# Optimization experiments

Measured on AMD Instinct MI355X. Metric: run time of the kernel, lower is better.

Reference implementation:

```python
import jax, jax.numpy as jnp
import numpy as np

N = 100000       # nodes
E = 3200000      # edges (before self-loops)
F_IN = 256       # input feature dim
HID = 32         # GCNConv output dim
CLASSES = 10


def setup_inputs() -> dict:
    key = jax.random.key(0)
    k1, k2, k3, k4 = jax.random.split(key, 4)
    feature = jax.random.normal(k1, (N, F_IN), dtype=jnp.float32)
    edge_index = jax.random.randint(k2, (2, E), 0, N, dtype=jnp.int64)
    W1 = jax.random.normal(k3, (F_IN, HID), dtype=jnp.float32) * (1.0 / np.sqrt(F_IN))
    b1 = jnp.zeros((HID,), dtype=jnp.float32)
    W2 = jax.random.normal(k4, (HID, CLASSES), dtype=jnp.float32) * (1.0 / np.sqrt(HID))
    b2 = jnp.zeros((CLASSES,), dtype=jnp.float32)
    return {"feature": feature, "edge_index": edge_index,
            "W1": W1, "b1": b1, "W2": W2, "b2": b2}


def reference(feature, edge_index, W1, b1, W2, b2):
    # --- GCNConv(features, 32): PyG semantics ---
    # add self-loops
    loops = jnp.arange(N, dtype=edge_index.dtype)
    row = jnp.concatenate([edge_index[0], loops])   # source nodes
    col = jnp.concatenate([edge_index[1], loops])   # target nodes
    # linear transform before propagation
    h = feature @ W1                                # [N, HID]
    # symmetric deg^{-1/2} normalization (degree counted at targets)
    deg = jax.ops.segment_sum(jnp.ones_like(col, dtype=h.dtype), col,
                              num_segments=N)       # [N], >=1 due to self-loops
    dinv = jax.lax.rsqrt(deg)
    norm = dinv[row] * dinv[col]                    # [E+N]
    # gather-scale-scatter aggregation
    msg = h[row] * norm[:, None]                    # [E+N, HID]
    agg = jax.ops.segment_sum(msg, col, num_segments=N) + b1  # [N, HID]
    # --- relu, (dropout: identity in eval), final linear, log_softmax ---
    act = jax.nn.relu(agg)
    logits = act @ W2 + b2                          # [N, CLASSES]
    return jax.nn.log_softmax(logits, axis=1)
```

## Files before the change

### kernel.cpp

```cpp
#include <hip/hip_runtime.h>

constexpr int N_NODES = 100000;
constexpr int E_EDGES = 3200000;
constexpr int F_IN    = 256;
constexpr int HID     = 32;
constexpr int NCLS    = 10;

constexpr int BUCK_SHIFT = 7;
constexpr int NPB        = 128;
constexpr int NBUCK      = (N_NODES + NPB - 1) / NPB;
constexpr int EPB        = 4096;
constexpr int NBLK1      = (E_EDGES + EPB - 1) / EPB;
constexpr int CAP        = 6144;

constexpr size_t OFF_FLAG = 0;
constexpr size_t OFF_GCUR = 4u << 10;
constexpr size_t OFF_BB   = 8u << 10;
constexpr size_t OFF_W1F  = 32u << 10;
constexpr size_t OFF_CNT  = 4u << 20;
constexpr size_t OFF_OFF  = 5u << 20;
constexpr size_t OFF_DINV = 6u << 20;
constexpr size_t OFF_CSR  = 7u << 20;
constexpr size_t OFF_BIN  = 20u << 20;
constexpr size_t OFF_HS   = 20u << 20;

typedef __attribute__((ext_vector_type(8))) short bf16x8;
typedef __attribute__((ext_vector_type(4))) float f32x4;

__device__ __forceinline__ unsigned pack_bf16x2(float a, float b) {
    unsigned ua = __float_as_uint(a), ub = __float_as_uint(b);
    ua = (ua + 0x7FFFu + ((ua >> 16) & 1u)) >> 16;
    ub = (ub + 0x7FFFu + ((ub >> 16) & 1u)) >> 16;
    return ua | (ub << 16);
}
__device__ __forceinline__ unsigned short bf16_rne(float x) {
    unsigned u = __float_as_uint(x);
    return (unsigned short)((u + 0x7FFFu + ((u >> 16) & 1u)) >> 16);
}
__device__ __forceinline__ float bf16_lo(unsigned p) { return __uint_as_float(p << 16); }
__device__ __forceinline__ float bf16_hi(unsigned p) { return __uint_as_float(p & 0xFFFF0000u); }

__device__ __forceinline__ int load_idx(const void* ei, long long i, int is64) {
    if (is64) return (int)((const long long*)ei)[i];
    return ((const int*)ei)[i];
}

__global__ __launch_bounds__(1024) void k_init(const int* __restrict__ ei32,
                                               int* __restrict__ flag,
                                               int* __restrict__ gcur) {
    __shared__ int nz;
    int tid = threadIdx.x;
    if (tid == 0) nz = 0;
    __syncthreads();
    if (tid < 1024) {
        if (ei32[2 * tid + 1] != 0) atomicOr(&nz, 1);
    }
    __syncthreads();
    if (tid == 0) flag[0] = (nz == 0) ? 1 : 0;
    if (tid < NBUCK) gcur[tid] = tid * CAP;
}

__global__ void k_w1frag(const float* __restrict__ W1, unsigned* __restrict__ w1f) {
    int tid = threadIdx.x;
    for (int i = tid; i < 16 * 64 * 4; i += 256) {
        int p    = i & 3;
        int lane = (i >> 2) & 63;
        int f    = i >> 8;
        int ks = f >> 1, t = f & 1;
        int kg = lane >> 4, col = lane & 15;
        int k0 = ks * 32 + kg * 8 + p * 2;
        float w0 = W1[k0 * HID + t * 16 + col];
        float w1 = W1[(k0 + 1) * HID + t * 16 + col];
        w1f[i] = pack_bf16x2(w0, w1);
    }
}

__global__ __launch_bounds__(1024) void k_scat(const void* __restrict__ ei,
                                               const int* __restrict__ flag,
                                               int* __restrict__ gcur,
                                               unsigned* __restrict__ binned) {
    __shared__ unsigned       sval[EPB];
    __shared__ unsigned short sbuck[EPB];
    __shared__ int h[NBUCK];
    __shared__ int cur[NBUCK];
    int tid = threadIdx.x, blk = blockIdx.x;
    for (int i = tid; i < NBUCK; i += 1024) h[i] = 0;
    __syncthreads();

    int is64 = flag[0];
    int base = blk * EPB;
    int nedge = min(EPB, E_EDGES - base);
    for (int k = tid; k < nedge; k += 1024) {
        int i = base + k;
        int r = load_idx(ei, i, is64);
        int c = load_idx(ei, (long long)E_EDGES + i, is64);
        int b = c >> BUCK_SHIFT;
        sval[k]  = ((unsigned)r << BUCK_SHIFT) | ((unsigned)c & (NPB - 1));
        sbuck[k] = (unsigned short)b;
        atomicAdd(&h[b], 1);
    }
    __syncthreads();

    for (int j = tid; j < NBUCK; j += 1024) {
        int c = h[j];
        cur[j] = (c > 0) ? atomicAdd(&gcur[j], c) : 0;
    }
    __syncthreads();

    for (int k = tid; k < nedge; k += 1024) {
        int d = atomicAdd(&cur[sbuck[k]], 1);
        binned[d] = sval[k];
    }
}

__global__ __launch_bounds__(1024) void k_bscan(const int* __restrict__ gcur,
                                                int* __restrict__ bucketBase) {
    __shared__ int s[1024];
    int tid = threadIdx.x;
    int v = (tid < NBUCK) ? (gcur[tid] - tid * CAP) : 0;
    s[tid] = v;
    __syncthreads();
    for (int d = 1; d < 1024; d <<= 1) {
        int t = (tid >= d) ? s[tid - d] : 0;
        __syncthreads();
        s[tid] += t;
        __syncthreads();
    }
    if (tid < NBUCK) bucketBase[tid] = s[tid] - v;
    if (tid == 1023) bucketBase[NBUCK] = s[1023];
}

__global__ __launch_bounds__(256) void k_p2(const unsigned* __restrict__ binned,
                                            const int* __restrict__ gcur,
                                            const int* __restrict__ bucketBase,
                                            int* __restrict__ cnt,
                                            int* __restrict__ off,
                                            float* __restrict__ dinv,
                                            int* __restrict__ csr) {
    __shared__ int lcnt[NPB], sc[NPB], lcur[NPB];
    int b = blockIdx.x, tid = threadIdx.x;
    int s = b * CAP, e = gcur[b];
    int db = bucketBase[b];
    if (tid < NPB) lcnt[tid] = 0;
    __syncthreads();
    for (int i = s + tid; i < e; i += 256)
        atomicAdd(&lcnt[binned[i] & (NPB - 1)], 1);
    __syncthreads();
    if (tid < NPB) sc[tid] = lcnt[tid];
    __syncthreads();
    for (int d = 1; d < NPB; d <<= 1) {
        int t = 0;
        if (tid < NPB && tid >= d) t = sc[tid - d];
        __syncthreads();
        if (tid < NPB) sc[tid] += t;
        __syncthreads();
    }
    if (tid < NPB) {
        int o = db + sc[tid] - lcnt[tid];
        lcur[tid] = o;
        int node = b * NPB + tid;
        if (node < N_NODES) {
            off[node]  = o;
            cnt[node]  = lcnt[tid];
            dinv[node] = rsqrtf((float)lcnt[tid] + 1.0f);
        }
    }
    __syncthreads();
    for (int i = s + tid; i < e; i += 256) {
        unsigned p = binned[i];
        int pos = atomicAdd(&lcur[p & (NPB - 1)], 1);
        csr[pos] = (int)(p >> BUCK_SHIFT);
    }
}

__global__ __launch_bounds__(256) void k_h(const float* __restrict__ feat,
                                           const unsigned* __restrict__ w1f,
                                           const float* __restrict__ dinv,
                                           unsigned short* __restrict__ hs16s) {
    int tid  = threadIdx.x;
    int lane = tid & 63;
    long wid = (long)blockIdx.x * 4 + (tid >> 6);
    int n0 = (int)(wid * 16);
    if (n0 >= N_NODES) return;

    bf16x8 bfrag[16];
    const bf16x8* wv = (const bf16x8*)w1f;
    #pragma unroll
    for (int f = 0; f < 16; f++) bfrag[f] = wv[f * 64 + lane];

    int arow = lane & 15;
    int kg   = lane >> 4;
    const float4* fr = (const float4*)(feat + (size_t)(n0 + arow) * F_IN);

    f32x4 acc0 = {0.f, 0.f, 0.f, 0.f};
    f32x4 acc1 = {0.f, 0.f, 0.f, 0.f};

    #pragma unroll
    for (int ks = 0; ks < 8; ks++) {
        float4 fa = fr[ks * 8 + kg * 2 + 0];
        float4 fb = fr[ks * 8 + kg * 2 + 1];
        unsigned au[4];
        au[0] = pack_bf16x2(fa.x, fa.y);
        au[1] = pack_bf16x2(fa.z, fa.w);
        au[2] = pack_bf16x2(fb.x, fb.y);
        au[3] = pack_bf16x2(fb.z, fb.w);
        bf16x8 af = *(bf16x8*)au;
        acc0 = __builtin_amdgcn_mfma_f32_16x16x32_bf16(af, bfrag[ks * 2 + 0], acc0, 0, 0, 0);
        acc1 = __builtin_amdgcn_mfma_f32_16x16x32_bf16(af, bfrag[ks * 2 + 1], acc1, 0, 0, 0);
    }

    int rb = kg * 4;
    #pragma unroll
    for (int r = 0; r < 4; r++) {
        int node = n0 + rb + r;
        float di = dinv[node];
        hs16s[(size_t)node * HID + arow]      = bf16_rne(acc0[r] * di);
        hs16s[(size_t)node * HID + 16 + arow] = bf16_rne(acc1[r] * di);
    }
}

__global__ __launch_bounds__(256) void k_aggout(const int* __restrict__ off,
                                                const int* __restrict__ cnt,
                                                const int* __restrict__ csr,
                                                const unsigned* __restrict__ hs16,
                                                const float* __restrict__ dinv,
                                                const float* __restrict__ b1,
                                                const float* __restrict__ W2,
                                                const float* __restrict__ b2,
                                                float* __restrict__ out) {
    __shared__ float W2s[HID * NCLS];
    __shared__ float b2s[NCLS];
    int tid = threadIdx.x;
    for (int i = tid; i < HID * NCLS; i += 256) W2s[i] = W2[i];
    if (tid < NCLS) b2s[tid] = b2[tid];
    __syncthreads();

    int j2   = tid & 15;
    int g    = tid >> 4;
    int node = blockIdx.x * 16 + g;

    int o = off[node];
    int n = cnt[node];

    unsigned ps = hs16[(size_t)node * 16 + j2];
    float acc0 = bf16_lo(ps), acc1 = bf16_hi(ps);

    int i = 0;
    for (; i + 4 <= n; i += 4) {
        int r0 = csr[o + i + 0];
        int r1 = csr[o + i + 1];
        int r2 = csr[o + i + 2];
        int r3 = csr[o + i + 3];
        unsigned p0 = hs16[(size_t)r0 * 16 + j2];
        unsigned p1 = hs16[(size_t)r1 * 16 + j2];
        unsigned p2 = hs16[(size_t)r2 * 16 + j2];
        unsigned p3 = hs16[(size_t)r3 * 16 + j2];
        acc0 += (bf16_lo(p0) + bf16_lo(p1)) + (bf16_lo(p2) + bf16_lo(p3));
        acc1 += (bf16_hi(p0) + bf16_hi(p1)) + (bf16_hi(p2) + bf16_hi(p3));
    }
    for (; i < n; i++) {
        unsigned p = hs16[(size_t)csr[o + i] * 16 + j2];
        acc0 += bf16_lo(p);
        acc1 += bf16_hi(p);
    }

    float di = dinv[node];
    float a0 = fmaxf(b1[2 * j2 + 0] + acc0 * di, 0.f);
    float a1 = fmaxf(b1[2 * j2 + 1] + acc1 * di, 0.f);

    float p[NCLS];
    #pragma unroll
    for (int c = 0; c < NCLS; c++)
        p[c] = a0 * W2s[(2 * j2 + 0) * NCLS + c] + a1 * W2s[(2 * j2 + 1) * NCLS + c];

    #pragma unroll
    for (int d = 1; d < 16; d <<= 1) {
        #pragma unroll
        for (int c = 0; c < NCLS; c++) p[c] += __shfl_xor(p[c], d, 16);
    }

    #pragma unroll
    for (int c = 0; c < NCLS; c++) p[c] += b2s[c];
    float m = p[0];
    #pragma unroll
    for (int c = 1; c < NCLS; c++) m = fmaxf(m, p[c]);
    float se = 0.f;
    #pragma unroll
    for (int c = 0; c < NCLS; c++) se += expf(p[c] - m);
    float lse = m + logf(se);

    if (j2 < NCLS) {
        float myv = p[0];
        #pragma unroll
        for (int c = 1; c < NCLS; c++) myv = (j2 == c) ? p[c] : myv;
        out[(size_t)node * NCLS + j2] = myv - lse;
    }
}

extern "C" void kernel_launch(void* const* d_in, const int* in_sizes, int n_in,
                              void* d_out, int out_size, void* d_ws, size_t ws_size,
                              hipStream_t stream) {
    const float* feat = (const float*)d_in[0];
    const void*  ei   = d_in[1];
    const float* W1   = (const float*)d_in[2];
    const float* b1   = (const float*)d_in[3];
    const float* W2   = (const float*)d_in[4];
    const float* b2   = (const float*)d_in[5];
    float* out = (float*)d_out;

    char* ws = (char*)d_ws;
    int*      flag   = (int*)(ws + OFF_FLAG);
    int*      gcur   = (int*)(ws + OFF_GCUR);
    int*      bbase  = (int*)(ws + OFF_BB);
    unsigned* w1f    = (unsigned*)(ws + OFF_W1F);
    int*      cnt    = (int*)(ws + OFF_CNT);
    int*      off    = (int*)(ws + OFF_OFF);
    float*    dinv   = (float*)(ws + OFF_DINV);
    int*      csr    = (int*)(ws + OFF_CSR);
    unsigned* binned = (unsigned*)(ws + OFF_BIN);
    unsigned* hs16   = (unsigned*)(ws + OFF_HS);

    k_init<<<1, 1024, 0, stream>>>((const int*)ei, flag, gcur);
    k_w1frag<<<1, 256, 0, stream>>>(W1, w1f);
    k_scat<<<NBLK1, 1024, 0, stream>>>(ei, flag, gcur, binned);
    k_bscan<<<1, 1024, 0, stream>>>(gcur, bbase);
    k_p2<<<NBUCK, 256, 0, stream>>>(binned, gcur, bbase, cnt, off, dinv, csr);

    k_h<<<(N_NODES / 16 + 3) / 4, 256, 0, stream>>>(feat, w1f, dinv,
                                                    (unsigned short*)hs16);
    k_aggout<<<N_NODES / 16, 256, 0, stream>>>(off, cnt, csr, hs16, dinv,
                                               b1, W2, b2, out);
}
```

Before: 143.2 us.

## Vectorize aggregation gathers to 16-byte loads with 4 lanes per node

The aggregation kernel now assigns 4 lanes per node, each gathering a uint4 (8 bf16 features) per neighbour, instead of 16 lanes each loading 4 bytes. Each block therefore handles 64 nodes rather than 16, and the cross-lane reduction for the output layer shrinks to 2 shuffle steps. This cuts the number of gather instructions and raises per-lane memory-level parallelism, at the cost of more registers and fewer threads per node. Separately, the edge-scatter block size is doubled to 8192 edges and the CSR build kernel uses 512 threads.

```diff
diff --git a/kernel.cpp b/kernel.cpp
--- a/kernel.cpp
+++ b/kernel.cpp
@@ -9,7 +9,7 @@
 constexpr int BUCK_SHIFT = 7;
 constexpr int NPB        = 128;
 constexpr int NBUCK      = (N_NODES + NPB - 1) / NPB;
-constexpr int EPB        = 4096;
+constexpr int EPB        = 8192;
 constexpr int NBLK1      = (E_EDGES + EPB - 1) / EPB;
 constexpr int CAP        = 6144;
 
@@ -52,9 +52,7 @@
     int tid = threadIdx.x;
     if (tid == 0) nz = 0;
     __syncthreads();
-    if (tid < 1024) {
-        if (ei32[2 * tid + 1] != 0) atomicOr(&nz, 1);
-    }
+    if (ei32[2 * tid + 1] != 0) atomicOr(&nz, 1);
     __syncthreads();
     if (tid == 0) flag[0] = (nz == 0) ? 1 : 0;
     if (tid < NBUCK) gcur[tid] = tid * CAP;
@@ -130,7 +128,7 @@
     if (tid == 1023) bucketBase[NBUCK] = s[1023];
 }
 
-__global__ __launch_bounds__(256) void k_p2(const unsigned* __restrict__ binned,
+__global__ __launch_bounds__(512) void k_p2(const unsigned* __restrict__ binned,
                                             const int* __restrict__ gcur,
                                             const int* __restrict__ bucketBase,
                                             int* __restrict__ cnt,
@@ -143,7 +141,7 @@
     int db = bucketBase[b];
     if (tid < NPB) lcnt[tid] = 0;
     __syncthreads();
-    for (int i = s + tid; i < e; i += 256)
+    for (int i = s + tid; i < e; i += 512)
         atomicAdd(&lcnt[binned[i] & (NPB - 1)], 1);
     __syncthreads();
     if (tid < NPB) sc[tid] = lcnt[tid];
@@ -166,7 +164,7 @@
         }
     }
     __syncthreads();
-    for (int i = s + tid; i < e; i += 256) {
+    for (int i = s + tid; i < e; i += 512) {
         unsigned p = binned[i];
         int pos = atomicAdd(&lcur[p & (NPB - 1)], 1);
         csr[pos] = (int)(p >> BUCK_SHIFT);
@@ -235,15 +233,24 @@
     if (tid < NCLS) b2s[tid] = b2[tid];
     __syncthreads();
 
-    int j2   = tid & 15;
-    int g    = tid >> 4;
-    int node = blockIdx.x * 16 + g;
+    int l2   = tid & 3;
+    int g    = tid >> 2;
+    int node = blockIdx.x * 64 + g;
+    if (node >= N_NODES) return;
 
     int o = off[node];
     int n = cnt[node];
 
-    unsigned ps = hs16[(size_t)node * 16 + j2];
-    float acc0 = bf16_lo(ps), acc1 = bf16_hi(ps);
+    const uint4* hsv = (const uint4*)hs16;
+    uint4 ps = hsv[(size_t)node * 4 + l2];
+    float a0 = bf16_lo(ps.x), a1 = bf16_hi(ps.x);
+    float a2 = bf16_lo(ps.y), a3 = bf16_hi(ps.y);
+    float a4 = bf16_lo(ps.z), a5 = bf16_hi(ps.z);
+    float a6 = bf16_lo(ps.w), a7 = bf16_hi(ps.w);
+
+    #define ADDQ(Q) \
+        a0 += bf16_lo(Q.x); a1 += bf16_hi(Q.x); a2 += bf16_lo(Q.y); a3 += bf16_hi(Q.y); \
+        a4 += bf16_lo(Q.z); a5 += bf16_hi(Q.z); a6 += bf16_lo(Q.w); a7 += bf16_hi(Q.w);
 
     int i = 0;
     for (; i + 4 <= n; i += 4) {
@@ -251,32 +258,44 @@
         int r1 = csr[o + i + 1];
         int r2 = csr[o + i + 2];
         int r3 = csr[o + i + 3];
-        unsigned p0 = hs16[(size_t)r0 * 16 + j2];
-        unsigned p1 = hs16[(size_t)r1 * 16 + j2];
-        unsigned p2 = hs16[(size_t)r2 * 16 + j2];
-        unsigned p3 = hs16[(size_t)r3 * 16 + j2];
-        acc0 += (bf16_lo(p0) + bf16_lo(p1)) + (bf16_lo(p2) + bf16_lo(p3));
-        acc1 += (bf16_hi(p0) + bf16_hi(p1)) + (bf16_hi(p2) + bf16_hi(p3));
+        uint4 q0 = hsv[(size_t)r0 * 4 + l2];
+        uint4 q1 = hsv[(size_t)r1 * 4 + l2];
+        uint4 q2 = hsv[(size_t)r2 * 4 + l2];
+        uint4 q3 = hsv[(size_t)r3 * 4 + l2];
+        ADDQ(q0) ADDQ(q1) ADDQ(q2) ADDQ(q3)
     }
     for (; i < n; i++) {
-        unsigned p = hs16[(size_t)csr[o + i] * 16 + j2];
-        acc0 += bf16_lo(p);
-        acc1 += bf16_hi(p);
-    }
+        uint4 q = hsv[(size_t)csr[o + i] * 4 + l2];
+        ADDQ(q)
+    }
+    #undef ADDQ
 
     float di = dinv[node];
-    float a0 = fmaxf(b1[2 * j2 + 0] + acc0 * di, 0.f);
-    float a1 = fmaxf(b1[2 * j2 + 1] + acc1 * di, 0.f);
+    float4 b1lo = *(const float4*)(b1 + 8 * l2);
+    float4 b1hi = *(const float4*)(b1 + 8 * l2 + 4);
+    float act[8];
+    act[0] = fmaxf(b1lo.x + a0 * di, 0.f);
+    act[1] = fmaxf(b1lo.y + a1 * di, 0.f);
+    act[2] = fmaxf(b1lo.z + a2 * di, 0.f);
+    act[3] = fmaxf(b1lo.w + a3 * di, 0.f);
+    act[4] = fmaxf(b1hi.x + a4 * di, 0.f);
+    act[5] = fmaxf(b1hi.y + a5 * di, 0.f);
+    act[6] = fmaxf(b1hi.z + a6 * di, 0.f);
+    act[7] = fmaxf(b1hi.w + a7 * di, 0.f);
 
     float p[NCLS];
     #pragma unroll
-    for (int c = 0; c < NCLS; c++)
-        p[c] = a0 * W2s[(2 * j2 + 0) * NCLS + c] + a1 * W2s[(2 * j2 + 1) * NCLS + c];
-
-    #pragma unroll
-    for (int d = 1; d < 16; d <<= 1) {
+    for (int c = 0; c < NCLS; c++) {
+        float s = 0.f;
         #pragma unroll
-        for (int c = 0; c < NCLS; c++) p[c] += __shfl_xor(p[c], d, 16);
+        for (int k = 0; k < 8; k++) s = fmaf(act[k], W2s[(8 * l2 + k) * NCLS + c], s);
+        p[c] = s;
+    }
+
+    #pragma unroll
+    for (int d = 1; d < 4; d <<= 1) {
+        #pragma unroll
+        for (int c = 0; c < NCLS; c++) p[c] += __shfl_xor(p[c], d, 4);
     }
 
     #pragma unroll
@@ -289,11 +308,15 @@
     for (int c = 0; c < NCLS; c++) se += expf(p[c] - m);
     float lse = m + logf(se);
 
-    if (j2 < NCLS) {
-        float myv = p[0];
-        #pragma unroll
-        for (int c = 1; c < NCLS; c++) myv = (j2 == c) ? p[c] : myv;
-        out[(size_t)node * NCLS + j2] = myv - lse;
+    #pragma unroll
+    for (int q = 0; q < 3; q++) {
+        int c = l2 + 4 * q;
+        if (c < NCLS) {
+            float v = p[0];
+            #pragma unroll
+            for (int cc = 1; cc < NCLS; cc++) v = (c == cc) ? p[cc] : v;
+            out[(size_t)node * NCLS + c] = v - lse;
+        }
     }
 }
 
@@ -324,10 +347,10 @@
     k_w1frag<<<1, 256, 0, stream>>>(W1, w1f);
     k_scat<<<NBLK1, 1024, 0, stream>>>(ei, flag, gcur, binned);
     k_bscan<<<1, 1024, 0, stream>>>(gcur, bbase);
-    k_p2<<<NBUCK, 256, 0, stream>>>(binned, gcur, bbase, cnt, off, dinv, csr);
+    k_p2<<<NBUCK, 512, 0, stream>>>(binned, gcur, bbase, cnt, off, dinv, csr);
 
     k_h<<<(N_NODES / 16 + 3) / 4, 256, 0, stream>>>(feat, w1f, dinv,
                                                     (unsigned short*)hs16);
-    k_aggout<<<N_NODES / 16, 256, 0, stream>>>(off, cnt, csr, hs16, dinv,
-                                               b1, W2, b2, out);
-}
+    k_aggout<<<(N_NODES + 63) / 64, 256, 0, stream>>>(off, cnt, csr, hs16, dinv,
+                                                      b1, W2, b2, out);
+}
```

Result: faster. 132.9 us (-7.2%).
